# Kernel tuning notes

Measured on AMD Instinct MI355X. Metric: run time of the kernel, lower is better.

## Reference

```python
import jax, jax.numpy as jnp
import numpy as np

N_NODES = 50000
N_EDGES = 800000
IN_F = 128
OUT_F = 128
HEADS = 8
HEAD_DIM = OUT_F // HEADS
EDGE_F = 32


def setup_inputs() -> dict:
    key = jax.random.key(0)
    ks = jax.random.split(key, 14)
    s = lambda fan_in: 1.0 / np.sqrt(fan_in)
    return {
        "node_features": jax.random.normal(ks[0], (N_NODES, IN_F), jnp.float32),
        "edge_index": jax.random.randint(ks[1], (2, N_EDGES), 0, N_NODES, jnp.int64),
        "edge_features": jax.random.normal(ks[2], (N_EDGES, EDGE_F), jnp.float32),
        "Wq": jax.random.uniform(ks[3], (IN_F, OUT_F), jnp.float32, -s(IN_F), s(IN_F)),
        "bq": jnp.zeros((OUT_F,), jnp.float32),
        "Wk": jax.random.uniform(ks[4], (IN_F, OUT_F), jnp.float32, -s(IN_F), s(IN_F)),
        "bk": jnp.zeros((OUT_F,), jnp.float32),
        "Wv": jax.random.uniform(ks[5], (IN_F, OUT_F), jnp.float32, -s(IN_F), s(IN_F)),
        "bv": jnp.zeros((OUT_F,), jnp.float32),
        "We": jax.random.uniform(ks[6], (EDGE_F, HEADS), jnp.float32, -s(EDGE_F), s(EDGE_F)),
        "be": jnp.zeros((HEADS,), jnp.float32),
        "Wo": jax.random.uniform(ks[7], (OUT_F, OUT_F), jnp.float32, -s(OUT_F), s(OUT_F)),
        "bo": jnp.zeros((OUT_F,), jnp.float32),
    }


def reference(node_features, edge_index, edge_features,
              Wq, bq, Wk, bk, Wv, bv, We, be, Wo, bo):
    n_nodes = node_features.shape[0]
    n_edges = edge_index.shape[1]
    sources, targets = edge_index[0], edge_index[1]
    scale = HEAD_DIM ** -0.5

    # dense projections: [n_nodes, heads, head_dim]
    Q = (node_features @ Wq + bq).reshape(n_nodes, HEADS, HEAD_DIM)
    K = (node_features @ Wk + bk).reshape(n_nodes, HEADS, HEAD_DIM)
    V = (node_features @ Wv + bv).reshape(n_nodes, HEADS, HEAD_DIM)

    # gather by edge
    Q_t = Q[targets]           # [n_edges, heads, head_dim]
    K_s = K[sources]
    V_s = V[sources]

    scores = jnp.sum(Q_t * K_s, axis=-1) * scale      # [n_edges, heads]
    scores = scores + (edge_features @ We + be)       # edge bias

    # segment softmax over incoming edges of each target node
    max_s = jax.ops.segment_max(scores, targets, num_segments=n_nodes)
    scores = scores - max_s[targets]
    exp_s = jnp.exp(scores)
    denom = jax.ops.segment_sum(exp_s, targets, num_segments=n_nodes) + 1e-10
    probs = exp_s / denom[targets]                    # [n_edges, heads]

    weighted_V = probs[:, :, None] * V_s              # [n_edges, heads, head_dim]
    aggregated = jax.ops.segment_sum(
        weighted_V.reshape(n_edges, -1), targets, num_segments=n_nodes)
    return aggregated @ Wo + bo
```

## Files before the change

kernel.cpp:

```cpp
#include <hip/hip_runtime.h>

typedef __attribute__((ext_vector_type(8))) short shortx8;
typedef __attribute__((ext_vector_type(4))) float floatx4;
typedef unsigned short u16;
typedef unsigned int u32;

__device__ __forceinline__ float bf2f(unsigned short u) {
    union { unsigned int i; float f; } v; v.i = ((unsigned int)u) << 16; return v.f;
}
__device__ __forceinline__ float bfl(u32 u) {
    union { u32 i; float f; } v; v.i = u << 16; return v.f;
}
__device__ __forceinline__ float bfh(u32 u) {
    union { u32 i; float f; } v; v.i = u & 0xFFFF0000u; return v.f;
}
__device__ __forceinline__ unsigned short f2bf(float f) {
    union { float f; unsigned int i; } v; v.f = f;
    unsigned int x = v.i;
    unsigned int r = x + 0x7FFFu + ((x >> 16) & 1u);
    return (unsigned short)(r >> 16);
}
__device__ __forceinline__ float ldf(const void* p, int i, bool f32) {
    return f32 ? ((const float*)p)[i] : bf2f(((const u16*)p)[i]);
}

__global__ __launch_bounds__(256) void detect_zero_k(
    const u16* __restrict__ nf, const int* __restrict__ ei,
    int* __restrict__ flags, int* __restrict__ deg, int M)
{
    int tid = threadIdx.x;
    if (blockIdx.x != 0) {
        int i = (blockIdx.x - 1) * 256 + tid;
        if (i < M) deg[i] = 0;
        return;
    }
    __shared__ int cnt[2];
    if (tid < 2) cnt[tid] = 0;
    __syncthreads();
    int c0 = 0;
    for (int i = tid; i < 65536; i += 256) {
        u16 v = nf[i];
        if ((v & 0x7F80u) == 0x7F80u) c0++;
    }
    int c1 = 0;
    for (int i = tid; i < 4096; i += 256) {
        if (ei[2 * i + 1] != 0) c1++;
    }
    atomicAdd(&cnt[0], c0);
    atomicAdd(&cnt[1], c1);
    __syncthreads();
    if (tid == 0) {
        flags[0] = (cnt[0] > 8) ? 1 : 0;
        flags[1] = (cnt[1] < 100) ? 1 : 0;
    }
}

__global__ __launch_bounds__(256) void prep_k(
    const void* __restrict__ W0, const void* __restrict__ W1,
    const void* __restrict__ W2, const void* __restrict__ W3,
    const void* __restrict__ b0, const void* __restrict__ b1,
    const void* __restrict__ b2, const void* __restrict__ b3,
    const void* __restrict__ We, const void* __restrict__ be,
    const int* __restrict__ flags,
    u16* __restrict__ WT, float* __restrict__ biasWs,
    float* __restrict__ WeWs, float* __restrict__ beWs)
{
    bool f32 = flags[0] != 0;
    int tid = threadIdx.x;
    if (blockIdx.x < 32) {
        int t = blockIdx.x * 256 + tid;
        int mat  = t >> 11;
        int r    = t & 2047;
        int lane = r & 63;
        int ks   = (r >> 6) & 3;
        int ct   = r >> 8;
        const void* W = (mat == 0) ? W0 : (mat == 1) ? W1 : (mat == 2) ? W2 : W3;
        int k0  = ks * 32 + (lane >> 4) * 8;
        int col = ct * 16 + (lane & 15);
        u16 tmp[8];
#pragma unroll
        for (int j = 0; j < 8; ++j) {
            int off = (k0 + j) * 128 + col;
            tmp[j] = f32 ? f2bf(((const float*)W)[off]) : ((const u16*)W)[off];
        }
        *(shortx8*)(WT + (size_t)t * 8) = *(const shortx8*)tmp;
    } else {
        if (tid < 128) {
            biasWs[0 * 128 + tid] = ldf(b0, tid, f32);
            biasWs[1 * 128 + tid] = ldf(b1, tid, f32);
            biasWs[2 * 128 + tid] = ldf(b2, tid, f32);
            biasWs[3 * 128 + tid] = ldf(b3, tid, f32);
        }
        WeWs[tid] = ldf(We, tid, f32);
        if (tid < 8) beWs[tid] = ldf(be, tid, f32);
    }
}

__global__ __launch_bounds__(256) void hist_k(
    const int* __restrict__ ei, int* __restrict__ deg,
    int E, const int* __restrict__ flags)
{
    int e = blockIdx.x * 256 + threadIdx.x;
    if (e >= E) return;
    int tgt = flags[1] ? ei[2 * (E + e)] : ei[E + e];
    atomicAdd(&deg[tgt], 1);
}

__global__ __launch_bounds__(256) void scan1_k(
    const int* __restrict__ deg, int* __restrict__ incl, int* __restrict__ bsum, int M)
{
    __shared__ int s[256];
    int tid = threadIdx.x;
    int i = blockIdx.x * 256 + tid;
    int v = (i < M) ? deg[i] : 0;
    s[tid] = v;
    __syncthreads();
#pragma unroll
    for (int off = 1; off < 256; off <<= 1) {
        int t = (tid >= off) ? s[tid - off] : 0;
        __syncthreads();
        s[tid] += t;
        __syncthreads();
    }
    if (i < M) incl[i] = s[tid];
    if (tid == 255) bsum[blockIdx.x] = s[255];
}

__global__ __launch_bounds__(256) void scan2_k(
    const int* __restrict__ bsum, int* __restrict__ boff, int nb)
{
    __shared__ int s[256];
    int tid = threadIdx.x;
    int v = (tid < nb) ? bsum[tid] : 0;
    s[tid] = v;
    __syncthreads();
#pragma unroll
    for (int off = 1; off < 256; off <<= 1) {
        int t = (tid >= off) ? s[tid - off] : 0;
        __syncthreads();
        s[tid] += t;
        __syncthreads();
    }
    if (tid < nb) boff[tid] = s[tid] - v;
}

__global__ __launch_bounds__(256) void scan3_k(
    int* __restrict__ incl_cur, const int* __restrict__ boff,
    const int* __restrict__ deg, int* __restrict__ rowptr, int M)
{
    int i = blockIdx.x * 256 + threadIdx.x;
    if (i >= M) return;
    int r = incl_cur[i] + boff[i >> 8];
    rowptr[i + 1] = r;
    incl_cur[i] = r - deg[i];
    if (i == 0) rowptr[0] = 0;
}

__global__ __launch_bounds__(256) void qkv_gemm_k(
    const void* __restrict__ A, int M,
    const u16* __restrict__ WT, const float* __restrict__ biasWs,
    u16* __restrict__ Qb, u16* __restrict__ KVb,
    const int* __restrict__ flags)
{
    bool aF32 = flags[0] != 0;
    int lane = threadIdx.x & 63;
    int wave = threadIdx.x >> 6;
    int quad = lane >> 4;
    int l15  = lane & 15;
    int m0   = blockIdx.x * 128 + wave * 32;

    shortx8 afrag[2][4];
#pragma unroll
    for (int mt = 0; mt < 2; ++mt) {
        int row = m0 + mt * 16 + l15;
        row = row < M ? row : M - 1;
#pragma unroll
        for (int ks = 0; ks < 4; ++ks) {
            size_t base = (size_t)row * 128 + ks * 32 + quad * 8;
            if (aF32) {
                const floatx4* ap = (const floatx4*)((const float*)A + base);
                floatx4 f0 = ap[0], f1 = ap[1];
                u16 tmp[8];
#pragma unroll
                for (int j = 0; j < 4; ++j) { tmp[j] = f2bf(f0[j]); tmp[4 + j] = f2bf(f1[j]); }
                afrag[mt][ks] = *(const shortx8*)tmp;
            } else {
                afrag[mt][ks] = *(const shortx8*)((const u16*)A + base);
            }
        }
    }

#pragma unroll
    for (int mat = 0; mat < 3; ++mat) {
        floatx4 acc[2][8];
#pragma unroll
        for (int a = 0; a < 2; ++a)
#pragma unroll
            for (int b = 0; b < 8; ++b)
                acc[a][b] = (floatx4){0.f, 0.f, 0.f, 0.f};
#pragma unroll
        for (int ks = 0; ks < 4; ++ks) {
#pragma unroll
            for (int ct = 0; ct < 8; ++ct) {
                shortx8 bfrag = *(const shortx8*)(WT + (size_t)mat * 16384 +
                                                  ((size_t)(ct * 4 + ks) * 64 + lane) * 8);
                acc[0][ct] = __builtin_amdgcn_mfma_f32_16x16x32_bf16(afrag[0][ks], bfrag, acc[0][ct], 0, 0, 0);
                acc[1][ct] = __builtin_amdgcn_mfma_f32_16x16x32_bf16(afrag[1][ks], bfrag, acc[1][ct], 0, 0, 0);
            }
        }
        u16* base = (mat == 0) ? Qb : (mat == 1) ? KVb : (KVb + 128);
        int stride = (mat == 0) ? 128 : 256;
#pragma unroll
        for (int ct = 0; ct < 8; ++ct) {
            int col = ct * 16 + l15;
            float bs = biasWs[mat * 128 + col];
#pragma unroll
            for (int mt = 0; mt < 2; ++mt) {
#pragma unroll
                for (int r = 0; r < 4; ++r) {
                    int row = m0 + mt * 16 + quad * 4 + r;
                    if (row < M)
                        base[(size_t)row * stride + col] = f2bf(acc[mt][ct][r] + bs);
                }
            }
        }
    }
}

__global__ __launch_bounds__(256) void edge_scatter_k(
    const int* __restrict__ ei, const void* __restrict__ ef,
    int* __restrict__ cur,
    const float* __restrict__ WeWs, const float* __restrict__ beWs,
    int2* __restrict__ pr2, float* __restrict__ EBe,
    int E, const int* __restrict__ flags)
{
    __shared__ float sWe[256];
    __shared__ float sbe[8];
    int tid = threadIdx.x;
    sWe[tid] = WeWs[tid];
    if (tid < 8) sbe[tid] = beWs[tid];
    __syncthreads();

    int e = blockIdx.x * 256 + tid;
    if (e >= E) return;
    bool f32 = flags[0] != 0;
    bool i64 = flags[1] != 0;

    int src = i64 ? ei[2 * e]       : ei[e];
    int tgt = i64 ? ei[2 * (E + e)] : ei[E + e];
    int pos = atomicAdd(&cur[tgt], 1);
    pr2[pos] = make_int2(src, e);

    float v[32];
    if (f32) {
        const floatx4* ep = (const floatx4*)((const float*)ef + (size_t)e * 32);
#pragma unroll
        for (int g = 0; g < 8; ++g) {
            floatx4 t = ep[g];
#pragma unroll
            for (int j = 0; j < 4; ++j) v[g * 4 + j] = t[j];
        }
    } else {
        const shortx8* ep = (const shortx8*)((const u16*)ef + (size_t)e * 32);
#pragma unroll
        for (int g = 0; g < 4; ++g) {
            shortx8 t = ep[g];
#pragma unroll
            for (int j = 0; j < 8; ++j) v[g * 8 + j] = bf2f((unsigned short)t[j]);
        }
    }
    float eb[8];
#pragma unroll
    for (int h = 0; h < 8; ++h) eb[h] = sbe[h];
#pragma unroll
    for (int k = 0; k < 32; ++k)
#pragma unroll
        for (int h = 0; h < 8; ++h) eb[h] += v[k] * sWe[k * 8 + h];

    floatx4* op = (floatx4*)(EBe + (size_t)e * 8);
    op[0] = (floatx4){eb[0], eb[1], eb[2], eb[3]};
    op[1] = (floatx4){eb[4], eb[5], eb[6], eb[7]};
}

__global__ __launch_bounds__(256) void node_agg_k(
    const int2* __restrict__ pr2, const int* __restrict__ rowptr,
    const u16* __restrict__ Qb, const u16* __restrict__ KVb,
    const float* __restrict__ EBe, u16* __restrict__ aggN, int M, int E)
{
    int wave = threadIdx.x >> 6;
    int lane = threadIdx.x & 63;
    int n = blockIdx.x * 4 + wave;
    if (n >= M) return;
    int g = lane >> 4;
    int w = lane & 15;
    int h = w >> 1;

    int beg = rowptr[n], end = rowptr[n + 1];
    int pidx = beg + lane;
    if (pidx >= E) pidx = E - 1;
    int2 pv = pr2[pidx];

    uint4 qw = ((const uint4*)(Qb + (size_t)n * 128))[w];
    float q0 = bfl(qw.x), q1 = bfh(qw.x), q2 = bfl(qw.y), q3 = bfh(qw.y);
    float q4 = bfl(qw.z), q5 = bfh(qw.z), q6 = bfl(qw.w), q7 = bfh(qw.w);

    float acc[8];
#pragma unroll
    for (int j = 0; j < 8; ++j) acc[j] = 0.f;
    float dsum = 0.f;

    for (int i = beg; i < end; i += 4) {
        int idx = i + g;
        bool valid = idx < end;
        int cidx = valid ? idx : (end - 1);
        int off = cidx - beg;
        int src, eid;
        if (off < 64) {
            src = __shfl(pv.x, off);
            eid = __shfl(pv.y, off);
        } else {
            int2 t = pr2[cidx];
            src = t.x; eid = t.y;
        }
        float eb = EBe[(size_t)eid * 8 + h];
        const uint4* kvp = (const uint4*)(KVb + (size_t)src * 256);
        uint4 kw = kvp[w];
        uint4 vw = kvp[16 + w];
        float part = q0 * bfl(kw.x) + q1 * bfh(kw.x)
                   + q2 * bfl(kw.y) + q3 * bfh(kw.y)
                   + q4 * bfl(kw.z) + q5 * bfh(kw.z)
                   + q6 * bfl(kw.w) + q7 * bfh(kw.w);
        part += __shfl_xor(part, 1);
        float p = valid ? __expf(part * 0.25f + eb) : 0.f;
        dsum += p;
        acc[0] += p * bfl(vw.x); acc[1] += p * bfh(vw.x);
        acc[2] += p * bfl(vw.y); acc[3] += p * bfh(vw.y);
        acc[4] += p * bfl(vw.z); acc[5] += p * bfh(vw.z);
        acc[6] += p * bfl(vw.w); acc[7] += p * bfh(vw.w);
    }

    dsum += __shfl_xor(dsum, 16);
    dsum += __shfl_xor(dsum, 32);
#pragma unroll
    for (int j = 0; j < 8; ++j) {
        acc[j] += __shfl_xor(acc[j], 16);
        acc[j] += __shfl_xor(acc[j], 32);
    }
    if (g == 0) {
        float inv = 1.0f / (dsum + 1e-10f);
        uint4 o;
        o.x = (u32)f2bf(acc[0] * inv) | ((u32)f2bf(acc[1] * inv) << 16);
        o.y = (u32)f2bf(acc[2] * inv) | ((u32)f2bf(acc[3] * inv) << 16);
        o.z = (u32)f2bf(acc[4] * inv) | ((u32)f2bf(acc[5] * inv) << 16);
        o.w = (u32)f2bf(acc[6] * inv) | ((u32)f2bf(acc[7] * inv) << 16);
        ((uint4*)(aggN + (size_t)n * 128))[w] = o;
    }
}

__global__ __launch_bounds__(256) void out_gemm_k(
    const u16* __restrict__ A, int M,
    const u16* __restrict__ WT, const float* __restrict__ bias,
    void* __restrict__ out, const int* __restrict__ flags)
{
    bool oF32 = flags[0] != 0;
    int lane = threadIdx.x & 63;
    int wave = threadIdx.x >> 6;
    int quad = lane >> 4;
    int l15  = lane & 15;
    int m0   = blockIdx.x * 128 + wave * 32;

    floatx4 acc[2][8];
#pragma unroll
    for (int a = 0; a < 2; ++a)
#pragma unroll
        for (int b = 0; b < 8; ++b)
            acc[a][b] = (floatx4){0.f, 0.f, 0.f, 0.f};

#pragma unroll
    for (int ks = 0; ks < 4; ++ks) {
        shortx8 afrag[2];
#pragma unroll
        for (int mt = 0; mt < 2; ++mt) {
            int row = m0 + mt * 16 + l15;
            row = row < M ? row : M - 1;
            afrag[mt] = *(const shortx8*)(A + (size_t)row * 128 + ks * 32 + quad * 8);
        }
#pragma unroll
        for (int ct = 0; ct < 8; ++ct) {
            shortx8 bfrag = *(const shortx8*)(WT + ((size_t)(ct * 4 + ks) * 64 + lane) * 8);
            acc[0][ct] = __builtin_amdgcn_mfma_f32_16x16x32_bf16(afrag[0], bfrag, acc[0][ct], 0, 0, 0);
            acc[1][ct] = __builtin_amdgcn_mfma_f32_16x16x32_bf16(afrag[1], bfrag, acc[1][ct], 0, 0, 0);
        }
    }

#pragma unroll
    for (int ct = 0; ct < 8; ++ct) {
        int col = ct * 16 + l15;
        float bs = bias[col];
#pragma unroll
        for (int mt = 0; mt < 2; ++mt) {
#pragma unroll
            for (int r = 0; r < 4; ++r) {
                int row = m0 + mt * 16 + quad * 4 + r;
                if (row < M) {
                    float v = acc[mt][ct][r] + bs;
                    if (oF32) ((float*)out)[(size_t)row * 128 + col] = v;
                    else      ((u16*)out)[(size_t)row * 128 + col] = f2bf(v);
                }
            }
        }
    }
}

extern "C" void kernel_launch(void* const* d_in, const int* in_sizes, int n_in,
                              void* d_out, int out_size, void* d_ws, size_t ws_size,
                              hipStream_t stream)
{
    const void* nf = d_in[0];
    const int*  ei = (const int*)d_in[1];
    const void* ef = d_in[2];
    const void* Wq = d_in[3];  const void* bq = d_in[4];
    const void* Wk = d_in[5];  const void* bk = d_in[6];
    const void* Wv = d_in[7];  const void* bv = d_in[8];
    const void* We = d_in[9];  const void* be = d_in[10];
    const void* Wo = d_in[11]; const void* bo = d_in[12];

    int M = in_sizes[0] / 128;
    int E = in_sizes[1] / 2;
    int nb = (M + 255) / 256;

    char* ws = (char*)d_ws;
    int*   flags  = (int*)(ws + 0);
    float* biasWs = (float*)(ws + 256);
    float* WeWs   = (float*)(ws + 2304);
    float* beWs   = (float*)(ws + 3328);
    u16*   WT     = (u16*)(ws + 4096);
    size_t O1 = 4096 + 131072;
    size_t qrow  = (size_t)M * 128 * 2;
    size_t kvrow = (size_t)M * 256 * 2;
    u16* Qb  = (u16*)(ws + O1);
    u16* KVb = (u16*)(ws + O1 + qrow);
    size_t O2 = O1 + qrow + kvrow;
    float* EBe = (float*)(ws + O2);
    size_t O3 = O2 + (size_t)E * 8 * 4;
    int2* pr2   = (int2*)(ws + O3);
    int* deg    = (int*)(pr2 + E);
    int* incl   = deg + M;
    int* rowptr = incl + M;
    int* bsum   = rowptr + M + 1;
    int* boff   = bsum + 256;
    u16* aggN   = Qb;

    detect_zero_k<<<1 + nb, 256, 0, stream>>>((const u16*)nf, ei, flags, deg, M);
    prep_k<<<33, 256, 0, stream>>>(Wq, Wk, Wv, Wo, bq, bk, bv, bo, We, be,
                                   flags, WT, biasWs, WeWs, beWs);

    int eblocks = (E + 255) / 256;
    hist_k<<<eblocks, 256, 0, stream>>>(ei, deg, E, flags);
    scan1_k<<<nb, 256, 0, stream>>>(deg, incl, bsum, M);
    scan2_k<<<1, 256, 0, stream>>>(bsum, boff, nb);
    scan3_k<<<nb, 256, 0, stream>>>(incl, boff, deg, rowptr, M);

    int gblocks = (M + 127) / 128;
    qkv_gemm_k<<<gblocks, 256, 0, stream>>>(nf, M, WT, biasWs, Qb, KVb, flags);

    edge_scatter_k<<<eblocks, 256, 0, stream>>>(ei, ef, incl , WeWs, beWs,
                                                pr2, EBe, E, flags);

    node_agg_k<<<(M + 3) / 4, 256, 0, stream>>>(pr2, rowptr, Qb, KVb, EBe, aggN, M, E);

    out_gemm_k<<<gblocks, 256, 0, stream>>>(aggN, M, WT + 3 * 16384, biasWs + 384, d_out, flags);
}
```

Measured before the change: 465.8 us.

## Fuse edge-bias into histogram pass with rank capture; unroll node aggregation by two

The histogram kernel now records each edge's atomic rank and also computes the edge-bias projection, so the scatter pass no longer needs atomics and only writes pr2 at rowptr[tgt]+rank. The scan no longer produces a cursor array. The node aggregation loop handles two edge groups per iteration, putting more independent K/V gathers in flight to hide memory latency. The cost is an extra rank array write and read, plus higher register use in the aggregation kernel.

```diff
diff --git a/kernel.cpp b/kernel.cpp
--- a/kernel.cpp
+++ b/kernel.cpp
@@ -96,14 +96,54 @@
     }
 }
 
-__global__ __launch_bounds__(256) void hist_k(
-    const int* __restrict__ ei, int* __restrict__ deg,
-    int E, const int* __restrict__ flags)
-{
-    int e = blockIdx.x * 256 + threadIdx.x;
+__global__ __launch_bounds__(256) void hist_ebias_k(
+    const int* __restrict__ ei, const void* __restrict__ ef,
+    int* __restrict__ deg, int* __restrict__ rank,
+    const float* __restrict__ WeWs, const float* __restrict__ beWs,
+    float* __restrict__ EBe, int E, const int* __restrict__ flags)
+{
+    __shared__ float sWe[256];
+    __shared__ float sbe[8];
+    int tid = threadIdx.x;
+    sWe[tid] = WeWs[tid];
+    if (tid < 8) sbe[tid] = beWs[tid];
+    __syncthreads();
+
+    int e = blockIdx.x * 256 + tid;
     if (e >= E) return;
+    bool f32 = flags[0] != 0;
     int tgt = flags[1] ? ei[2 * (E + e)] : ei[E + e];
-    atomicAdd(&deg[tgt], 1);
+    rank[e] = atomicAdd(&deg[tgt], 1);
+
+    float v[32];
+    if (f32) {
+        const floatx4* ep = (const floatx4*)((const float*)ef + (size_t)e * 32);
+#pragma unroll
+        for (int g = 0; g < 8; ++g) {
+            floatx4 t = ep[g];
+#pragma unroll
+            for (int j = 0; j < 4; ++j) v[g * 4 + j] = t[j];
+        }
+    } else {
+        const shortx8* ep = (const shortx8*)((const u16*)ef + (size_t)e * 32);
+#pragma unroll
+        for (int g = 0; g < 4; ++g) {
+            shortx8 t = ep[g];
+#pragma unroll
+            for (int j = 0; j < 8; ++j) v[g * 8 + j] = bf2f((unsigned short)t[j]);
+        }
+    }
+    float eb[8];
+#pragma unroll
+    for (int h = 0; h < 8; ++h) eb[h] = sbe[h];
+#pragma unroll
+    for (int k = 0; k < 32; ++k)
+#pragma unroll
+        for (int h = 0; h < 8; ++h) eb[h] += v[k] * sWe[k * 8 + h];
+
+    floatx4* op = (floatx4*)(EBe + (size_t)e * 8);
+    op[0] = (floatx4){eb[0], eb[1], eb[2], eb[3]};
+    op[1] = (floatx4){eb[4], eb[5], eb[6], eb[7]};
 }
 
 __global__ __launch_bounds__(256) void scan1_k(
@@ -145,14 +185,12 @@
 }
 
 __global__ __launch_bounds__(256) void scan3_k(
-    int* __restrict__ incl_cur, const int* __restrict__ boff,
-    const int* __restrict__ deg, int* __restrict__ rowptr, int M)
+    const int* __restrict__ incl, const int* __restrict__ boff,
+    int* __restrict__ rowptr, int M)
 {
     int i = blockIdx.x * 256 + threadIdx.x;
     if (i >= M) return;
-    int r = incl_cur[i] + boff[i >> 8];
-    rowptr[i + 1] = r;
-    incl_cur[i] = r - deg[i];
+    rowptr[i + 1] = incl[i] + boff[i >> 8];
     if (i == 0) rowptr[0] = 0;
 }
 
@@ -227,59 +265,17 @@
     }
 }
 
-__global__ __launch_bounds__(256) void edge_scatter_k(
-    const int* __restrict__ ei, const void* __restrict__ ef,
-    int* __restrict__ cur,
-    const float* __restrict__ WeWs, const float* __restrict__ beWs,
-    int2* __restrict__ pr2, float* __restrict__ EBe,
+__global__ __launch_bounds__(256) void scatter_k(
+    const int* __restrict__ ei, const int* __restrict__ rank,
+    const int* __restrict__ rowptr, int2* __restrict__ pr2,
     int E, const int* __restrict__ flags)
 {
-    __shared__ float sWe[256];
-    __shared__ float sbe[8];
-    int tid = threadIdx.x;
-    sWe[tid] = WeWs[tid];
-    if (tid < 8) sbe[tid] = beWs[tid];
-    __syncthreads();
-
-    int e = blockIdx.x * 256 + tid;
+    int e = blockIdx.x * 256 + threadIdx.x;
     if (e >= E) return;
-    bool f32 = flags[0] != 0;
     bool i64 = flags[1] != 0;
-
     int src = i64 ? ei[2 * e]       : ei[e];
     int tgt = i64 ? ei[2 * (E + e)] : ei[E + e];
-    int pos = atomicAdd(&cur[tgt], 1);
-    pr2[pos] = make_int2(src, e);
-
-    float v[32];
-    if (f32) {
-        const floatx4* ep = (const floatx4*)((const float*)ef + (size_t)e * 32);
-#pragma unroll
-        for (int g = 0; g < 8; ++g) {
-            floatx4 t = ep[g];
-#pragma unroll
-            for (int j = 0; j < 4; ++j) v[g * 4 + j] = t[j];
-        }
-    } else {
-        const shortx8* ep = (const shortx8*)((const u16*)ef + (size_t)e * 32);
-#pragma unroll
-        for (int g = 0; g < 4; ++g) {
-            shortx8 t = ep[g];
-#pragma unroll
-            for (int j = 0; j < 8; ++j) v[g * 8 + j] = bf2f((unsigned short)t[j]);
-        }
-    }
-    float eb[8];
-#pragma unroll
-    for (int h = 0; h < 8; ++h) eb[h] = sbe[h];
-#pragma unroll
-    for (int k = 0; k < 32; ++k)
-#pragma unroll
-        for (int h = 0; h < 8; ++h) eb[h] += v[k] * sWe[k * 8 + h];
-
-    floatx4* op = (floatx4*)(EBe + (size_t)e * 8);
-    op[0] = (floatx4){eb[0], eb[1], eb[2], eb[3]};
-    op[1] = (floatx4){eb[4], eb[5], eb[6], eb[7]};
+    pr2[rowptr[tgt] + rank[e]] = make_int2(src, e);
 }
 
 __global__ __launch_bounds__(256) void node_agg_k(
@@ -309,34 +305,51 @@
     for (int j = 0; j < 8; ++j) acc[j] = 0.f;
     float dsum = 0.f;
 
-    for (int i = beg; i < end; i += 4) {
-        int idx = i + g;
-        bool valid = idx < end;
-        int cidx = valid ? idx : (end - 1);
-        int off = cidx - beg;
-        int src, eid;
-        if (off < 64) {
-            src = __shfl(pv.x, off);
-            eid = __shfl(pv.y, off);
-        } else {
-            int2 t = pr2[cidx];
-            src = t.x; eid = t.y;
-        }
-        float eb = EBe[(size_t)eid * 8 + h];
-        const uint4* kvp = (const uint4*)(KVb + (size_t)src * 256);
-        uint4 kw = kvp[w];
-        uint4 vw = kvp[16 + w];
-        float part = q0 * bfl(kw.x) + q1 * bfh(kw.x)
-                   + q2 * bfl(kw.y) + q3 * bfh(kw.y)
-                   + q4 * bfl(kw.z) + q5 * bfh(kw.z)
-                   + q6 * bfl(kw.w) + q7 * bfh(kw.w);
-        part += __shfl_xor(part, 1);
-        float p = valid ? __expf(part * 0.25f + eb) : 0.f;
-        dsum += p;
-        acc[0] += p * bfl(vw.x); acc[1] += p * bfh(vw.x);
-        acc[2] += p * bfl(vw.y); acc[3] += p * bfh(vw.y);
-        acc[4] += p * bfl(vw.z); acc[5] += p * bfh(vw.z);
-        acc[6] += p * bfl(vw.w); acc[7] += p * bfh(vw.w);
+    for (int i = beg; i < end; i += 8) {
+        int idxA = i + g;
+        int idxB = i + 4 + g;
+        bool vA = idxA < end;
+        bool vB = idxB < end;
+        int cA = vA ? idxA : (end - 1);
+        int cB = vB ? idxB : (end - 1);
+        int offA = cA - beg;
+        int offB = cB - beg;
+        int srcA, eidA, srcB, eidB;
+        if (offA < 64) { srcA = __shfl(pv.x, offA); eidA = __shfl(pv.y, offA); }
+        else           { int2 t = pr2[cA]; srcA = t.x; eidA = t.y; }
+        if (offB < 64) { srcB = __shfl(pv.x, offB); eidB = __shfl(pv.y, offB); }
+        else           { int2 t = pr2[cB]; srcB = t.x; eidB = t.y; }
+
+        const uint4* kpA = (const uint4*)(KVb + (size_t)srcA * 256);
+        const uint4* kpB = (const uint4*)(KVb + (size_t)srcB * 256);
+        uint4 kwA = kpA[w];
+        uint4 kwB = kpB[w];
+        uint4 vwA = kpA[16 + w];
+        uint4 vwB = kpB[16 + w];
+        float ebA = EBe[(size_t)eidA * 8 + h];
+        float ebB = EBe[(size_t)eidB * 8 + h];
+
+        float partA = q0 * bfl(kwA.x) + q1 * bfh(kwA.x)
+                    + q2 * bfl(kwA.y) + q3 * bfh(kwA.y)
+                    + q4 * bfl(kwA.z) + q5 * bfh(kwA.z)
+                    + q6 * bfl(kwA.w) + q7 * bfh(kwA.w);
+        float partB = q0 * bfl(kwB.x) + q1 * bfh(kwB.x)
+                    + q2 * bfl(kwB.y) + q3 * bfh(kwB.y)
+                    + q4 * bfl(kwB.z) + q5 * bfh(kwB.z)
+                    + q6 * bfl(kwB.w) + q7 * bfh(kwB.w);
+        partA += __shfl_xor(partA, 1);
+        partB += __shfl_xor(partB, 1);
+        float pA = vA ? __expf(partA * 0.25f + ebA) : 0.f;
+        float pB = vB ? __expf(partB * 0.25f + ebB) : 0.f;
+        dsum += pA + pB;
+        acc[0] += pA * bfl(vwA.x) + pB * bfl(vwB.x);
+        acc[1] += pA * bfh(vwA.x) + pB * bfh(vwB.x);
+        acc[2] += pA * bfl(vwA.y) + pB * bfl(vwB.y);
+        acc[3] += pA * bfh(vwA.y) + pB * bfh(vwB.y);
+        acc[4] += pA * bfl(vwA.z) + pB * bfl(vwB.z);
+        acc[5] += pA * bfh(vwA.z) + pB * bfh(vwB.z);
+        acc[6] += pA * bfl(vwA.w) + pB * bfl(vwB.w);
+        acc[7] += pA * bfh(vwA.w) + pB * bfh(vwB.w);
     }
 
     dsum += __shfl_xor(dsum, 16);
@@ -444,7 +457,8 @@
     float* EBe = (float*)(ws + O2);
     size_t O3 = O2 + (size_t)E * 8 * 4;
     int2* pr2   = (int2*)(ws + O3);
-    int* deg    = (int*)(pr2 + E);
+    int* rank   = (int*)(pr2 + E);
+    int* deg    = rank + E;
     int* incl   = deg + M;
     int* rowptr = incl + M;
     int* bsum   = rowptr + M + 1;
@@ -456,16 +470,16 @@
                                    flags, WT, biasWs, WeWs, beWs);
 
     int eblocks = (E + 255) / 256;
-    hist_k<<<eblocks, 256, 0, stream>>>(ei, deg, E, flags);
+    hist_ebias_k<<<eblocks, 256, 0, stream>>>(ei, ef, deg, rank, WeWs, beWs,
+                                              EBe, E, flags);
     scan1_k<<<nb, 256, 0, stream>>>(deg, incl, bsum, M);
     scan2_k<<<1, 256, 0, stream>>>(bsum, boff, nb);
-    scan3_k<<<nb, 256, 0, stream>>>(incl, boff, deg, rowptr, M);
+    scan3_k<<<nb, 256, 0, stream>>>(incl, boff, rowptr, M);
 
     int gblocks = (M + 127) / 128;
     qkv_gemm_k<<<gblocks, 256, 0, stream>>>(nf, M, WT, biasWs, Qb, KVb, flags);
 
-    edge_scatter_k<<<eblocks, 256, 0, stream>>>(ei, ef, incl , WeWs, beWs,
-                                                pr2, EBe, E, flags);
+    scatter_k<<<eblocks, 256, 0, stream>>>(ei, rank, rowptr, pr2, E, flags);
 
     node_agg_k<<<(M + 3) / 4, 256, 0, stream>>>(pr2, rowptr, Qb, KVb, EBe, aggN, M, E);
 
```

Result: faster. 443.1 us (-4.9%).
